# Kernel optimization log

Measured on AMD Instinct MI355X. Metric: run time of the kernel, lower is better.

Reference implementation:

```python
import jax, jax.numpy as jnp
import numpy as np
import math

B, N, D = 2, 192, 256

def _linear_params(key, d_in, d_out):
    kw, kb = jax.random.split(key)
    scale = 1.0 / math.sqrt(d_in)
    W = jax.random.uniform(kw, (d_out, d_in), jnp.float32, -scale, scale)
    b = jax.random.uniform(kb, (d_out,), jnp.float32, -scale, scale)
    return W, b

def setup_inputs() -> dict:
    key = jax.random.key(0)
    ks = jax.random.split(key, 7)
    Edges = jax.random.normal(ks[0], (B, N * N, D), jnp.float32)
    Wq_w, Wq_b = _linear_params(ks[1], D, D)
    Wk_w, Wk_b = _linear_params(ks[2], D, D)
    Wv_w, Wv_b = _linear_params(ks[3], D, D)
    Wb_w, Wb_b = _linear_params(ks[4], D, 1)
    Wg_w, Wg_b = _linear_params(ks[5], D, D)
    Wo_w, Wo_b = _linear_params(ks[6], D, D)
    return {"Edges": Edges, "Wq_w": Wq_w, "Wq_b": Wq_b, "Wk_w": Wk_w, "Wk_b": Wk_b,
            "Wv_w": Wv_w, "Wv_b": Wv_b, "Wb_w": Wb_w, "Wb_b": Wb_b,
            "Wg_w": Wg_w, "Wg_b": Wg_b, "Wo_w": Wo_w, "Wo_b": Wo_b}

def reference(Edges, Wq_w, Wq_b, Wk_w, Wk_b, Wv_w, Wv_b, Wb_w, Wb_b, Wg_w, Wg_b, Wo_w, Wo_b):
    # Edges: [B, N*N, D]; dropout is identity in eval mode.
    Bb, NN, Dd = Edges.shape
    n = int(round(math.sqrt(NN)))
    q = (Edges @ Wq_w.T + Wq_b).reshape(Bb, n, n, Dd)
    k = (Edges @ Wk_w.T + Wk_b).reshape(Bb, n, n, Dd)
    v = (Edges @ Wv_w.T + Wv_b).reshape(Bb, n, n, Dd)
    bmat = (Edges @ Wb_w.T + Wb_b).reshape(Bb, n, n)          # b[b,i,l]
    g = jax.nn.sigmoid(Edges @ Wg_w.T + Wg_b)                  # [B, N*N, D]
    # row attention: q(i,j) . k(i,l) ; column attention: q(i,j) . k(l,j)
    scores = (jnp.einsum('bijd,bild->bijl', q, k)
              + jnp.einsum('bijd,bljd->bijl', q, k)) / math.sqrt(Dd)
    sym_bias = bmat + jnp.swapaxes(bmat, 1, 2)                 # b[i,l] + b[l,i]
    alpha = jax.nn.softmax(scores + sym_bias[:, :, None, :], axis=-1)  # [B,n,n,n]
    # first value contraction along rows; second term matches torch's
    # transpose-free add: out2[b,i,j,d] = sum_l alpha[b,j,i,l] v[b,l,i,d]
    o1 = jnp.einsum('bijl,bild->bijd', alpha, v)
    o2 = jnp.einsum('bjil,blid->bijd', alpha, v)
    out = g * (o1 + o2).reshape(Bb, NN, Dd)
    out = jax.nn.relu(out @ Wo_w.T + Wo_b)
    return out
```

## Files before the change

### kernel.cpp

```cpp
#include <hip/hip_runtime.h>
#include <hip/hip_bf16.h>

typedef __hip_bfloat16 bf16;
typedef unsigned short u16;
typedef __attribute__((ext_vector_type(8))) short bf16x8;
typedef __attribute__((ext_vector_type(4))) float f32x4;

#define NB   2
#define NG   192
#define DD   256
#define NN2  (NG*NG)
#define MT   (NB*NN2)

static __device__ __forceinline__ float bfu2f(u16 u){
    return __uint_as_float(((unsigned)u) << 16);
}
static __device__ __forceinline__ u16 f2bfu(float f){
    bf16 h = __float2bfloat16(f);
    return *(u16*)&h;
}

static __device__ __forceinline__ void gl_lds16(const void* g, void* l){
    __builtin_amdgcn_global_load_lds(
        (const __attribute__((address_space(1))) unsigned int*)g,
        (__attribute__((address_space(3))) unsigned int*)l, 16, 0, 0);
}
static __device__ __forceinline__ int swz3(int x){ return ((x ^ (x>>3)) & 7) << 3; }

__global__ __launch_bounds__(256) void k_cast_eb(
    const float* __restrict__ E, const float* __restrict__ Wb,
    const float* __restrict__ bb, u16* __restrict__ Eb, float* __restrict__ bm)
{
    const int t = threadIdx.x;
    size_t base = (size_t)blockIdx.x*2048 + t*8;
    float4 x = *(const float4*)(E+base);
    float4 y = *(const float4*)(E+base+4);
    ushort4 a; a.x=f2bfu(x.x); a.y=f2bfu(x.y); a.z=f2bfu(x.z); a.w=f2bfu(x.w);
    ushort4 b; b.x=f2bfu(y.x); b.y=f2bfu(y.y); b.z=f2bfu(y.z); b.w=f2bfu(y.w);
    *(ushort4*)(Eb+base)   = a;
    *(ushort4*)(Eb+base+4) = b;
    const int l32 = t & 31;
    float4 w0 = ((const float4*)Wb)[l32*2];
    float4 w1 = ((const float4*)Wb)[l32*2+1];
    float s = x.x*w0.x + x.y*w0.y + x.z*w0.z + x.w*w0.w
            + y.x*w1.x + y.y*w1.y + y.z*w1.z + y.w*w1.w;
    #pragma unroll
    for (int off=1; off<32; off<<=1) s += __shfl_xor(s, off);
    if (l32 == 0) bm[blockIdx.x*8 + (t>>5)] = s + bb[0];
}

__global__ __launch_bounds__(256) void k_cast_w(
    const float* __restrict__ Wq, const float* __restrict__ Wk,
    const float* __restrict__ Wv, const float* __restrict__ Wg,
    const float* __restrict__ Wo,
    const float* __restrict__ bq, const float* __restrict__ bk,
    const float* __restrict__ bv, const float* __restrict__ bg,
    u16* __restrict__ Wcat, u16* __restrict__ Wob, float* __restrict__ biascat)
{
    int e = blockIdx.x*256 + threadIdx.x;
    Wcat[e]          = f2bfu(Wq[e]);
    Wcat[65536 + e]  = f2bfu(Wk[e]);
    Wcat[131072 + e] = f2bfu(Wv[e]);
    Wcat[196608 + e] = f2bfu(Wg[e]);
    Wob[e]           = f2bfu(Wo[e]);
    if (e < 1024){
        int p = e>>8, r = e&255;
        const float* bp = p==0?bq : p==1?bk : p==2?bv : bg;
        biascat[e] = bp[r];
    }
}

__global__ __launch_bounds__(256) void k_bias_sym(
    const float* __restrict__ bm, float* __restrict__ biassym)
{
    int rem = blockIdx.x*256 + threadIdx.x;
    int b = blockIdx.y;
    int i = rem / NG, l = rem % NG;
    biassym[(size_t)b*NN2 + rem] = bm[(size_t)b*NN2 + rem] + bm[(size_t)b*NN2 + l*NG + i];
}

static __device__ __forceinline__ void gemm128_dbuf(
    const u16* __restrict__ A, const u16* __restrict__ B,
    u16* As, u16* Bs, f32x4 acc[4][4], int t)
{
    const int lane = t & 63, w = t >> 6;
    const int wm = (w>>1)*64, wn = (w&1)*64;
    int offA[4], offB[4];
    #pragma unroll
    for (int f=0; f<4; f++){
        int ra = wm + f*16 + (lane&15);
        offA[f] = ra*32 + (((lane>>4) ^ ((ra>>1)&3)) << 3);
        int rb = wn + f*16 + (lane&15);
        offB[f] = rb*32 + (((lane>>4) ^ ((rb>>1)&3)) << 3);
    }
    auto stage = [&](int buf, int k0){
        #pragma unroll
        for (int it=0; it<2; it++){
            int c = it*256 + t;
            int row = c >> 2;
            int ks  = (c&3) ^ ((row>>1)&3);
            gl_lds16(A + (size_t)row*DD + k0 + ks*8, As + buf*4096 + c*8);
            gl_lds16(B + (size_t)row*DD + k0 + ks*8, Bs + buf*4096 + c*8);
        }
    };
    stage(0, 0);
    for (int ks=0; ks<8; ks++){
        if (ks<7){
            stage((ks+1)&1, (ks+1)*32);
            asm volatile("s_waitcnt vmcnt(4)" ::: "memory");
        } else {
            asm volatile("s_waitcnt vmcnt(0)" ::: "memory");
        }
        __builtin_amdgcn_s_barrier();
        const u16* Ab = As + (ks&1)*4096;
        const u16* Bb = Bs + (ks&1)*4096;
        bf16x8 a[4], b[4];
        #pragma unroll
        for (int f=0; f<4; f++) a[f] = *(const bf16x8*)(Ab + offA[f]);
        #pragma unroll
        for (int f=0; f<4; f++) b[f] = *(const bf16x8*)(Bb + offB[f]);
        #pragma unroll
        for (int mf=0; mf<4; mf++)
            #pragma unroll
            for (int nf=0; nf<4; nf++)
                acc[mf][nf] = __builtin_amdgcn_mfma_f32_16x16x32_bf16(a[mf], b[nf], acc[mf][nf], 0, 0, 0);
        __builtin_amdgcn_s_barrier();
    }
}

__global__ __launch_bounds__(256) void k_proj_mfma(
    const u16* __restrict__ Eb, const u16* __restrict__ Wcat,
    const float* __restrict__ biascat,
    u16* __restrict__ qb, u16* __restrict__ kb,
    u16* __restrict__ vb, u16* __restrict__ gb)
{
    __shared__ u16 As[2*4096];
    __shared__ u16 Bs[2*4096];
    const int blk = blockIdx.x;
    const int xj = blk & 7, xi = blk >> 3;
    const int m0 = (xj*72 + (xi>>3)) * 128;
    const int n0 = (xi & 7) * 128;
    const int t = threadIdx.x, lane = t&63, w = t>>6;
    f32x4 acc[4][4];
    #pragma unroll
    for (int i=0;i<4;i++)
        #pragma unroll
        for (int j=0;j<4;j++) acc[i][j] = f32x4{0.f,0.f,0.f,0.f};
    gemm128_dbuf(Eb + (size_t)m0*DD, Wcat + (size_t)n0*DD, As, Bs, acc, t);

    const int p = n0 >> 8;
    u16* outp = p==0?qb : p==1?kb : p==2?vb : gb;
    const int wm = (w>>1)*64, wn = (w&1)*64;
    #pragma unroll
    for (int mf=0; mf<4; mf++){
        int m = m0 + wm + mf*16 + (lane>>4)*4;
        #pragma unroll
        for (int nf=0; nf<4; nf++){
            int gn = n0 + wn + nf*16 + (lane&15);
            float bias = biascat[gn];
            int col = gn & 255;
            #pragma unroll
            for (int r=0; r<4; r++){
                float v = acc[mf][nf][r] + bias;
                if (p==3) v = 1.0f/(1.0f+__expf(-v));
                outp[(size_t)(m+r)*DD + col] = f2bfu(v);
            }
        }
    }
}

__global__ __launch_bounds__(256) void k_final_mfma(
    const u16* __restrict__ hb, const u16* __restrict__ Wob,
    const float* __restrict__ bo, float* __restrict__ out)
{
    __shared__ u16 As[2*4096];
    __shared__ u16 Bs[2*4096];
    const int blk = blockIdx.x;
    const int xj = blk & 7, xi = blk >> 3;
    const int m0 = (xj*72 + (xi>>1)) * 128;
    const int n0 = (xi & 1) * 128;
    const int t = threadIdx.x, lane = t&63, w = t>>6;
    f32x4 acc[4][4];
    #pragma unroll
    for (int i=0;i<4;i++)
        #pragma unroll
        for (int j=0;j<4;j++) acc[i][j] = f32x4{0.f,0.f,0.f,0.f};
    gemm128_dbuf(hb + (size_t)m0*DD, Wob + (size_t)n0*DD, As, Bs, acc, t);

    const int wm = (w>>1)*64, wn = (w&1)*64;
    #pragma unroll
    for (int mf=0; mf<4; mf++){
        int m = m0 + wm + mf*16 + (lane>>4)*4;
        #pragma unroll
        for (int nf=0; nf<4; nf++){
            int n = n0 + wn + nf*16 + (lane&15);
            float bias = bo[n];
            #pragma unroll
            for (int r=0; r<4; r++)
                out[(size_t)(m+r)*DD + n] = fmaxf(acc[mf][nf][r] + bias, 0.0f);
        }
    }
}

template<int MODE>
__global__ __launch_bounds__(512, 2) void k_scores(
    const u16* __restrict__ q, const u16* __restrict__ kmat,
    u16* __restrict__ outS)
{
    __shared__ u16 As[2][NG*64];
    __shared__ u16 Bs[2][NG*64];
    const int z = blockIdx.x, b = z/NG, r = z%NG;
    const int t = threadIdx.x, lane = t&63, w = t>>6;
    const int wm = (w&3)*48, wn = (w>>2)*96;
    const size_t astr = MODE ? (size_t)NG*DD : (size_t)DD;
    const u16* Ab = MODE ? q    + ((size_t)b*NN2 + r)*DD : q    + ((size_t)b*NG + r)*NG*DD;
    const u16* Bb = MODE ? kmat + ((size_t)b*NN2 + r)*DD : kmat + ((size_t)b*NG + r)*NG*DD;

    f32x4 acc[3][6];
    #pragma unroll
    for (int i=0;i<3;i++)
        #pragma unroll
        for (int j=0;j<6;j++) acc[i][j] = f32x4{0.f,0.f,0.f,0.f};

    int offA[3], offB[6];
    #pragma unroll
    for (int mf=0; mf<3; mf++){
        int x = wm + mf*16 + (lane&15);
        offA[mf] = x*64 + (((lane>>4)<<3) ^ swz3(x));
    }
    #pragma unroll
    for (int nf=0; nf<6; nf++){
        int x = wn + nf*16 + (lane&15);
        offB[nf] = x*64 + (((lane>>4)<<3) ^ swz3(x));
    }

    auto stage = [&](int buf, int k0){
        #pragma unroll
        for (int rr=0; rr<3; rr++){
            int c = t + rr*512;
            int x = c>>3, l8e = (c&7)<<3;
            size_t ro = (size_t)x*astr + k0;
            gl_lds16(Ab + ro + (l8e ^ swz3(x)), &As[buf][c*8]);
            gl_lds16(Bb + ro + (l8e ^ swz3(x)), &Bs[buf][c*8]);
        }
    };

    stage(0, 0);
    for (int ks=0; ks<4; ks++){
        if (ks<3){
            stage((ks+1)&1, (ks+1)*64);
            asm volatile("s_waitcnt vmcnt(6)" ::: "memory");
        } else {
            asm volatile("s_waitcnt vmcnt(0)" ::: "memory");
        }
        __builtin_amdgcn_s_barrier();
        const u16* A = &As[ks&1][0];
        const u16* B = &Bs[ks&1][0];
        #pragma unroll
        for (int kk=0; kk<2; kk++){
            bf16x8 a[3];
            #pragma unroll
            for (int mf=0; mf<3; mf++) a[mf] = *(const bf16x8*)(A + (offA[mf]^(kk<<5)));
            #pragma unroll
            for (int nf=0; nf<6; nf++){
                bf16x8 bf = *(const bf16x8*)(B + (offB[nf]^(kk<<5)));
                #pragma unroll
                for (int mf=0; mf<3; mf++)
                    acc[mf][nf] = __builtin_amdgcn_mfma_f32_16x16x32_bf16(a[mf], bf, acc[mf][nf], 0, 0, 0);
            }
        }
        __builtin_amdgcn_s_barrier();
    }

    u16* outb = outS + ((size_t)b*NG + r)*NN2;
    #pragma unroll
    for (int mf=0; mf<3; mf++){
        #pragma unroll
        for (int nf=0; nf<6; nf++){
            int lcol = wn + nf*16 + (lane&15);
            #pragma unroll
            for (int r4=0; r4<4; r4++){
                int x = wm + mf*16 + (lane>>4)*4 + r4;
                outb[(size_t)x*NG + lcol] = f2bfu(acc[mf][nf][r4]*0.0625f);
            }
        }
    }
}

__global__ __launch_bounds__(256) void k_softmax(
    const u16* __restrict__ S1, const u16* __restrict__ S2T,
    const float* __restrict__ biassym,
    u16* __restrict__ alpha, u16* __restrict__ alphaT)
{
    int rr   = blockIdx.x*4 + (threadIdx.x >> 6);
    int lane = threadIdx.x & 63;
    int b = blockIdx.y;
    int i = rr / NG, j = rr % NG;
    const u16* r1 = S1  + ((size_t)b*NN2 + rr)*NG;
    const u16* r2 = S2T + ((size_t)b*NN2 + (size_t)j*NG + i)*NG;
    const float* bs = biassym + ((size_t)b*NG + i)*NG;
    float vals[3];
    float mx = -1e30f;
    #pragma unroll
    for (int tt=0; tt<3; tt++){
        int l = lane + tt*64;
        float s = bfu2f(r1[l]) + bfu2f(r2[l]) + bs[l];
        vals[tt] = s;
        mx = fmaxf(mx, s);
    }
    #pragma unroll
    for (int off=32; off; off>>=1) mx = fmaxf(mx, __shfl_xor(mx, off));
    float sum = 0.f;
    #pragma unroll
    for (int tt=0; tt<3; tt++){ vals[tt] = __expf(vals[tt]-mx); sum += vals[tt]; }
    #pragma unroll
    for (int off=32; off; off>>=1) sum += __shfl_xor(sum, off);
    float inv = 1.0f/sum;
    u16* arow1 = alpha  + ((size_t)b*NN2 + rr)*NG;
    u16* arow2 = alphaT + ((size_t)b*NN2 + (size_t)j*NG + i)*NG;
    #pragma unroll
    for (int tt=0; tt<3; tt++){
        u16 vq = f2bfu(vals[tt]*inv);
        arow1[lane + tt*64] = vq;
        arow2[lane + tt*64] = vq;
    }
}

__global__ __launch_bounds__(512, 4) void k_attnout(
    const u16* __restrict__ alpha, const u16* __restrict__ alphaT,
    const u16* __restrict__ vb, const u16* __restrict__ gb, u16* __restrict__ hb)
{
    __shared__ u16 AsL[2][NG*64];
    __shared__ u16 Vs[128*64];
    const int z = blockIdx.x, bi = z>>1, dh = z&1;
    const int b = bi/NG, i = bi%NG;
    const int dbase = dh*128;
    const int t = threadIdx.x, lane = t&63, w = t>>6;
    const int wm = (w&1)*96, wn = (w>>1)*32;

    const u16* Abase0 = alpha  + (size_t)bi*NN2;
    const u16* Abase1 = alphaT + (size_t)bi*NN2;
    const u16* V0 = vb + (size_t)bi*NG*DD + dbase;
    const u16* V1 = vb + ((size_t)b*NG*NG + i)*DD + dbase;

    f32x4 acc[6][2];
    #pragma unroll
    for (int m=0;m<6;m++)
        #pragma unroll
        for (int n=0;n<2;n++) acc[m][n] = f32x4{0.f,0.f,0.f,0.f};

    int offA[6], offB[2];
    #pragma unroll
    for (int mf=0; mf<6; mf++){
        int j = wm + mf*16 + (lane&15);
        offA[mf] = j*64 + (((lane>>4)<<3) ^ swz3(j));
    }
    #pragma unroll
    for (int nf=0; nf<2; nf++){
        int d = wn + nf*16 + (lane&15);
        offB[nf] = d*64 + (((lane>>4)<<3) ^ swz3(d));
    }

    int4 vr[2];
    auto stageA = [&](int u, int buf){
        const u16* Ab = (u>=3) ? Abase1 : Abase0;
        int ls = (u>=3 ? u-3 : u)*64;
        #pragma unroll
        for (int rr=0; rr<3; rr++){
            int c = t + rr*512;
            int j = c>>3, l8e = (c&7)<<3;
            gl_lds16(Ab + (size_t)j*NG + ls + (l8e ^ swz3(j)), &AsL[buf][c*8]);
        }
    };
    auto loadV = [&](int u){
        int p = (u>=3), ls = (u>=3 ? u-3 : u)*64;
        #pragma unroll
        for (int rr=0; rr<2; rr++){
            int c = t + rr*512;
            int l = ls + (c>>4), d0 = (c&15)*8;
            const u16* src = p ? (V1 + (size_t)l*NG*DD + d0) : (V0 + (size_t)l*DD + d0);
            vr[rr] = *(const int4*)src;
        }
    };

    stageA(0, 0);
    loadV(0);
    for (int u=0; u<6; u++){
        #pragma unroll
        for (int rr=0; rr<2; rr++){
            int c = t + rr*512;
            int l = c>>4;
            l &= 63;
            int d0 = (c&15)*8, c3 = c&7;
            ushort* vp = (ushort*)&vr[rr];
            #pragma unroll
            for (int qd=0; qd<8; qd++)
                Vs[(d0+qd)*64 + (l ^ ((qd^c3)<<3))] = vp[qd];
        }
        if (u<5){ stageA(u+1, (u+1)&1); loadV(u+1); }
        asm volatile("s_waitcnt lgkmcnt(0)" ::: "memory");
        __builtin_amdgcn_s_barrier();
        const u16* A = &AsL[u&1][0];
        #pragma unroll
        for (int kk=0; kk<2; kk++){
            bf16x8 bfr[2];
            #pragma unroll
            for (int nf=0; nf<2; nf++) bfr[nf] = *(const bf16x8*)(Vs + (offB[nf]^(kk<<5)));
            #pragma unroll
            for (int mf=0; mf<6; mf++){
                bf16x8 afr = *(const bf16x8*)(A + (offA[mf]^(kk<<5)));
                acc[mf][0] = __builtin_amdgcn_mfma_f32_16x16x32_bf16(afr, bfr[0], acc[mf][0], 0, 0, 0);
                acc[mf][1] = __builtin_amdgcn_mfma_f32_16x16x32_bf16(afr, bfr[1], acc[mf][1], 0, 0, 0);
            }
        }
        __builtin_amdgcn_s_barrier();
    }

    #pragma unroll
    for (int mf=0; mf<6; mf++){
        #pragma unroll
        for (int nf=0; nf<2; nf++){
            #pragma unroll
            for (int r4=0; r4<4; r4++){
                int j = wm + mf*16 + (lane>>4)*4 + r4;
                int d = dbase + wn + nf*16 + (lane&15);
                size_t idx = ((size_t)bi*NG + j)*DD + d;
                hb[idx] = f2bfu(bfu2f(gb[idx]) * acc[mf][nf][r4]);
            }
        }
    }
}

extern "C" void kernel_launch(void* const* d_in, const int* in_sizes, int n_in,
                              void* d_out, int out_size, void* d_ws, size_t ws_size,
                              hipStream_t stream)
{
    const float* E  = (const float*)d_in[0];
    const float* Wq = (const float*)d_in[1];  const float* bq = (const float*)d_in[2];
    const float* Wk = (const float*)d_in[3];  const float* bk = (const float*)d_in[4];
    const float* Wv = (const float*)d_in[5];  const float* bv = (const float*)d_in[6];
    const float* Wb = (const float*)d_in[7];  const float* bb = (const float*)d_in[8];
    const float* Wg = (const float*)d_in[9];  const float* bg = (const float*)d_in[10];
    const float* Wo = (const float*)d_in[11]; const float* bo = (const float*)d_in[12];
    float* out = (float*)d_out;

    const size_t BF = (size_t)MT*DD*2;
    const size_t SC = (size_t)NB*NG*NG*NG*4;
    char* ws = (char*)d_ws;
    u16* Eb  = (u16*)ws;
    u16* S1  = (u16*)ws;
    u16* S2T = (u16*)(ws + SC/2);
    u16* hb  = (u16*)ws;
    u16* qb = (u16*)(ws + SC);           u16* alpha  = qb;
    u16* kb = (u16*)(ws + SC + BF);      u16* alphaT = kb;
    u16* vb = (u16*)(ws + SC + 2*BF);
    u16* gb = (u16*)(ws + SC + 3*BF);
    size_t tail = SC + 4*BF;
    float* bm      = (float*)(ws + tail); tail += (size_t)MT*4;
    float* biassym = (float*)(ws + tail); tail += (size_t)MT*4;
    u16* Wcat      = (u16*)(ws + tail);   tail += (size_t)1024*DD*2;
    u16* Wob       = (u16*)(ws + tail);   tail += (size_t)DD*DD*2;
    float* biascat = (float*)(ws + tail); tail += 1024*4;
    (void)ws_size;

    k_cast_w   <<<dim3(256), 256, 0, stream>>>(Wq,Wk,Wv,Wg,Wo, bq,bk,bv,bg, Wcat, Wob, biascat);
    k_cast_eb  <<<dim3(9216), 256, 0, stream>>>(E, Wb, bb, Eb, bm);
    k_proj_mfma<<<dim3(4608), 256, 0, stream>>>(Eb, Wcat, biascat, qb, kb, vb, gb);
    k_bias_sym <<<dim3(NN2/256, NB), 256, 0, stream>>>(bm, biassym);
    k_scores<0><<<dim3(NB*NG), 512, 0, stream>>>(qb, kb, S1);
    k_scores<1><<<dim3(NB*NG), 512, 0, stream>>>(qb, kb, S2T);
    k_softmax  <<<dim3(NN2/4, NB), 256, 0, stream>>>(S1, S2T, biassym, alpha, alphaT);
    k_attnout  <<<dim3(NB*NG*2), 512, 0, stream>>>(alpha, alphaT, vb, gb, hb);
    k_final_mfma<<<dim3(1152), 256, 0, stream>>>(hb, Wob, bo, out);
}
```

Baseline: 237.8 us.

## Use BK=64 GEMM staging and LDS-staged vectorized epilogue stores

Doubles the GEMM K-tile from 32 to 64 with an XOR-swizzled LDS layout, halving the number of barrier/wait iterations in the projection and final GEMMs. Epilogues of the projection, final and score kernels now write accumulator tiles to a per-wave LDS slab and read them back as rows, so global stores are 16-byte vectors instead of scattered 2- or 4-byte writes. Costs are doubled LDS use per block, which may lower occupancy, and extra LDS round trips in the epilogue.

```diff
diff --git a/kernel.cpp b/kernel.cpp
--- a/kernel.cpp
+++ b/kernel.cpp
@@ -26,6 +26,7 @@
         (__attribute__((address_space(3))) unsigned int*)l, 16, 0, 0);
 }
 static __device__ __forceinline__ int swz3(int x){ return ((x ^ (x>>3)) & 7) << 3; }
+static __device__ __forceinline__ int esw(int row){ return ((row>>2)&1)<<4; }
 
 __global__ __launch_bounds__(256) void k_cast_eb(
     const float* __restrict__ E, const float* __restrict__ Wb,
@@ -79,51 +80,59 @@
     biassym[(size_t)b*NN2 + rem] = bm[(size_t)b*NN2 + rem] + bm[(size_t)b*NN2 + l*NG + i];
 }
 
-static __device__ __forceinline__ void gemm128_dbuf(
+static __device__ __forceinline__ void gemm128_bk64(
     const u16* __restrict__ A, const u16* __restrict__ B,
     u16* As, u16* Bs, f32x4 acc[4][4], int t)
 {
     const int lane = t & 63, w = t >> 6;
     const int wm = (w>>1)*64, wn = (w&1)*64;
-    int offA[4], offB[4];
+    int rA[4], rB[4];
     #pragma unroll
     for (int f=0; f<4; f++){
-        int ra = wm + f*16 + (lane&15);
-        offA[f] = ra*32 + (((lane>>4) ^ ((ra>>1)&3)) << 3);
-        int rb = wn + f*16 + (lane&15);
-        offB[f] = rb*32 + (((lane>>4) ^ ((rb>>1)&3)) << 3);
-    }
+        rA[f] = wm + f*16 + (lane&15);
+        rB[f] = wn + f*16 + (lane&15);
+    }
+    const int q0 = lane>>4;
     auto stage = [&](int buf, int k0){
         #pragma unroll
-        for (int it=0; it<2; it++){
+        for (int it=0; it<4; it++){
             int c = it*256 + t;
-            int row = c >> 2;
-            int ks  = (c&3) ^ ((row>>1)&3);
-            gl_lds16(A + (size_t)row*DD + k0 + ks*8, As + buf*4096 + c*8);
-            gl_lds16(B + (size_t)row*DD + k0 + ks*8, Bs + buf*4096 + c*8);
+            int row = c >> 3, q = c & 7;
+            gl_lds16(A + (size_t)row*DD + k0 + ((q ^ (row&7))<<3), As + buf*8192 + c*8);
+        }
+        #pragma unroll
+        for (int it=0; it<4; it++){
+            int c = it*256 + t;
+            int row = c >> 3, q = c & 7;
+            gl_lds16(B + (size_t)row*DD + k0 + ((q ^ (row&7))<<3), Bs + buf*8192 + c*8);
         }
     };
     stage(0, 0);
-    for (int ks=0; ks<8; ks++){
-        if (ks<7){
-            stage((ks+1)&1, (ks+1)*32);
-            asm volatile("s_waitcnt vmcnt(4)" ::: "memory");
+    for (int ks=0; ks<4; ks++){
+        if (ks<3){
+            stage((ks+1)&1, (ks+1)*64);
+            asm volatile("s_waitcnt vmcnt(8)" ::: "memory");
         } else {
             asm volatile("s_waitcnt vmcnt(0)" ::: "memory");
         }
         __builtin_amdgcn_s_barrier();
-        const u16* Ab = As + (ks&1)*4096;
-        const u16* Bb = Bs + (ks&1)*4096;
-        bf16x8 a[4], b[4];
-        #pragma unroll
-        for (int f=0; f<4; f++) a[f] = *(const bf16x8*)(Ab + offA[f]);
-        #pragma unroll
-        for (int f=0; f<4; f++) b[f] = *(const bf16x8*)(Bb + offB[f]);
-        #pragma unroll
-        for (int mf=0; mf<4; mf++)
-            #pragma unroll
-            for (int nf=0; nf<4; nf++)
-                acc[mf][nf] = __builtin_amdgcn_mfma_f32_16x16x32_bf16(a[mf], b[nf], acc[mf][nf], 0, 0, 0);
+        const u16* Ab = As + (ks&1)*8192;
+        const u16* Bb = Bs + (ks&1)*8192;
+        #pragma unroll
+        for (int kk=0; kk<2; kk++){
+            const int G = kk*4 + q0;
+            bf16x8 a[4], b[4];
+            #pragma unroll
+            for (int f=0; f<4; f++){
+                a[f] = *(const bf16x8*)(Ab + rA[f]*64 + ((G ^ (rA[f]&7))<<3));
+                b[f] = *(const bf16x8*)(Bb + rB[f]*64 + ((G ^ (rB[f]&7))<<3));
+            }
+            #pragma unroll
+            for (int mf=0; mf<4; mf++)
+                #pragma unroll
+                for (int nf=0; nf<4; nf++)
+                    acc[mf][nf] = __builtin_amdgcn_mfma_f32_16x16x32_bf16(a[mf], b[nf], acc[mf][nf], 0, 0, 0);
+        }
         __builtin_amdgcn_s_barrier();
     }
 }
@@ -134,8 +143,8 @@
     u16* __restrict__ qb, u16* __restrict__ kb,
     u16* __restrict__ vb, u16* __restrict__ gb)
 {
-    __shared__ u16 As[2*4096];
-    __shared__ u16 Bs[2*4096];
+    __shared__ u16 As[2*8192];
+    __shared__ u16 Bs[2*8192];
     const int blk = blockIdx.x;
     const int xj = blk & 7, xi = blk >> 3;
     const int m0 = (xj*72 + (xi>>3)) * 128;
@@ -146,26 +155,44 @@
     for (int i=0;i<4;i++)
         #pragma unroll
         for (int j=0;j<4;j++) acc[i][j] = f32x4{0.f,0.f,0.f,0.f};
-    gemm128_dbuf(Eb + (size_t)m0*DD, Wcat + (size_t)n0*DD, As, Bs, acc, t);
+    gemm128_bk64(Eb + (size_t)m0*DD, Wcat + (size_t)n0*DD, As, Bs, acc, t);
 
     const int p = n0 >> 8;
     u16* outp = p==0?qb : p==1?kb : p==2?vb : gb;
     const int wm = (w>>1)*64, wn = (w&1)*64;
+    const int col0 = n0 & 255;
+    float* slab = (float*)As + w*1024;
     #pragma unroll
     for (int mf=0; mf<4; mf++){
-        int m = m0 + wm + mf*16 + (lane>>4)*4;
         #pragma unroll
         for (int nf=0; nf<4; nf++){
-            int gn = n0 + wn + nf*16 + (lane&15);
-            float bias = biascat[gn];
-            int col = gn & 255;
+            float bias = biascat[n0 + wn + nf*16 + (lane&15)];
             #pragma unroll
             for (int r=0; r<4; r++){
+                int row = (lane>>4)*4 + r;
+                int col = nf*16 + (lane&15);
                 float v = acc[mf][nf][r] + bias;
                 if (p==3) v = 1.0f/(1.0f+__expf(-v));
-                outp[(size_t)(m+r)*DD + col] = f2bfu(v);
-            }
-        }
+                slab[row*64 + (col ^ esw(row))] = v;
+            }
+        }
+        asm volatile("s_waitcnt lgkmcnt(0)" ::: "memory");
+        __builtin_amdgcn_sched_barrier(0);
+        #pragma unroll
+        for (int it2=0; it2<2; it2++){
+            int idx = it2*64 + lane;
+            int row = idx >> 3, colq = idx & 7;
+            const float* rp = slab + row*64;
+            int colx = (colq*8) ^ esw(row);
+            f32x4 v0 = *(const f32x4*)(rp + colx);
+            f32x4 v1 = *(const f32x4*)(rp + colx + 4);
+            u16 o[8];
+            o[0]=f2bfu(v0[0]); o[1]=f2bfu(v0[1]); o[2]=f2bfu(v0[2]); o[3]=f2bfu(v0[3]);
+            o[4]=f2bfu(v1[0]); o[5]=f2bfu(v1[1]); o[6]=f2bfu(v1[2]); o[7]=f2bfu(v1[3]);
+            int m = m0 + wm + mf*16 + row;
+            *(int4*)(outp + (size_t)m*DD + col0 + wn + colq*8) = *(int4*)o;
+        }
+        __builtin_amdgcn_sched_barrier(0);
     }
 }
 
@@ -173,8 +200,8 @@
     const u16* __restrict__ hb, const u16* __restrict__ Wob,
     const float* __restrict__ bo, float* __restrict__ out)
 {
-    __shared__ u16 As[2*4096];
-    __shared__ u16 Bs[2*4096];
+    __shared__ u16 As[2*8192];
+    __shared__ u16 Bs[2*8192];
     const int blk = blockIdx.x;
     const int xj = blk & 7, xi = blk >> 3;
     const int m0 = (xj*72 + (xi>>1)) * 128;
@@ -185,20 +212,34 @@
     for (int i=0;i<4;i++)
         #pragma unroll
         for (int j=0;j<4;j++) acc[i][j] = f32x4{0.f,0.f,0.f,0.f};
-    gemm128_dbuf(hb + (size_t)m0*DD, Wob + (size_t)n0*DD, As, Bs, acc, t);
+    gemm128_bk64(hb + (size_t)m0*DD, Wob + (size_t)n0*DD, As, Bs, acc, t);
 
     const int wm = (w>>1)*64, wn = (w&1)*64;
+    float* slab = (float*)As + w*1024;
     #pragma unroll
     for (int mf=0; mf<4; mf++){
-        int m = m0 + wm + mf*16 + (lane>>4)*4;
         #pragma unroll
         for (int nf=0; nf<4; nf++){
-            int n = n0 + wn + nf*16 + (lane&15);
-            float bias = bo[n];
-            #pragma unroll
-            for (int r=0; r<4; r++)
-                out[(size_t)(m+r)*DD + n] = fmaxf(acc[mf][nf][r] + bias, 0.0f);
-        }
+            float bias = bo[n0 + wn + nf*16 + (lane&15)];
+            #pragma unroll
+            for (int r=0; r<4; r++){
+                int row = (lane>>4)*4 + r;
+                int col = nf*16 + (lane&15);
+                slab[row*64 + (col ^ esw(row))] = fmaxf(acc[mf][nf][r] + bias, 0.0f);
+            }
+        }
+        asm volatile("s_waitcnt lgkmcnt(0)" ::: "memory");
+        __builtin_amdgcn_sched_barrier(0);
+        #pragma unroll
+        for (int it2=0; it2<4; it2++){
+            int idx = it2*64 + lane;
+            int row = idx >> 4, colq = idx & 15;
+            int colx = (colq*4) ^ esw(row);
+            f32x4 v = *(const f32x4*)(slab + row*64 + colx);
+            int m = m0 + wm + mf*16 + row;
+            *(f32x4*)(out + (size_t)m*DD + n0 + wn + colq*4) = v;
+        }
+        __builtin_amdgcn_sched_barrier(0);
     }
 }
 
@@ -273,17 +314,36 @@
     }
 
     u16* outb = outS + ((size_t)b*NG + r)*NN2;
+    float* slab = (w < 4) ? ((float*)&As[0][0] + w*1536)
+                          : ((float*)&Bs[0][0] + (w-4)*1536);
     #pragma unroll
     for (int mf=0; mf<3; mf++){
         #pragma unroll
         for (int nf=0; nf<6; nf++){
-            int lcol = wn + nf*16 + (lane&15);
             #pragma unroll
             for (int r4=0; r4<4; r4++){
-                int x = wm + mf*16 + (lane>>4)*4 + r4;
-                outb[(size_t)x*NG + lcol] = f2bfu(acc[mf][nf][r4]*0.0625f);
-            }
-        }
+                int row = (lane>>4)*4 + r4;
+                int col = nf*16 + (lane&15);
+                slab[row*96 + (col ^ esw(row))] = acc[mf][nf][r4]*0.0625f;
+            }
+        }
+        asm volatile("s_waitcnt lgkmcnt(0)" ::: "memory");
+        __builtin_amdgcn_sched_barrier(0);
+        #pragma unroll
+        for (int it2=0; it2<3; it2++){
+            int idx = it2*64 + lane;
+            int row = idx / 12, colq = idx % 12;
+            const float* rp = slab + row*96;
+            int colx = (colq*8) ^ esw(row);
+            f32x4 v0 = *(const f32x4*)(rp + colx);
+            f32x4 v1 = *(const f32x4*)(rp + colx + 4);
+            u16 o[8];
+            o[0]=f2bfu(v0[0]); o[1]=f2bfu(v0[1]); o[2]=f2bfu(v0[2]); o[3]=f2bfu(v0[3]);
+            o[4]=f2bfu(v1[0]); o[5]=f2bfu(v1[1]); o[6]=f2bfu(v1[2]); o[7]=f2bfu(v1[3]);
+            int x = wm + mf*16 + row;
+            *(int4*)(outb + (size_t)x*NG + wn + colq*8) = *(int4*)o;
+        }
+        __builtin_amdgcn_sched_barrier(0);
     }
 }
 
```

After: 249.7 us. 5.0% more time.
